# Performance work log

Hardware: AMD Instinct MI355X
Metric: run time of the kernel (lower is better)

## Reference

```python
import jax, jax.numpy as jnp
import numpy as np

B, T, D = 4, 2048, 1024
DK, DV = 1024, 1024
BETA1, BETA2 = 1.0, 1.0
EPS = 1e-12  # torch F.normalize eps


def setup_inputs() -> dict:
    key = jax.random.key(0)
    kx, kq, kk, kv, ko = jax.random.split(key, 5)
    def w(k, shape):
        return jax.random.normal(k, shape, dtype=jnp.float32) * (shape[0] ** -0.5)
    return {
        "x": jax.random.normal(kx, (B, T, D), dtype=jnp.float32),
        # Weights stored [in, out]; torch Linear is x @ W.T with W [out, in] -- equivalent math.
        "Wq": w(kq, (D, DK)),
        "Wk": w(kk, (D, DK)),
        "Wv": w(kv, (D, DV)),
        "Wo": w(ko, (DV, D)),
    }


def reference(x, Wq, Wk, Wv, Wo):
    scale = DK ** -0.5
    q = (x @ Wq) * scale                      # [B,T,DK]
    k = x @ Wk
    k = k / jnp.maximum(jnp.linalg.norm(k, axis=-1, keepdims=True), EPS)
    v = x @ Wv                                # [B,T,DV]
    # time-major for scan
    qT = jnp.swapaxes(q, 0, 1)
    kT = jnp.swapaxes(k, 0, 1)
    vT = jnp.swapaxes(v, 0, 1)
    S0 = jnp.zeros((B, DV, DK), dtype=x.dtype)

    def step(S, qkv_t):
        q_t, k_t, v_t = qkv_t                 # each [B, d]
        # S @ (I - b1 k k^T) = S - b1 (S k) k^T   (same math, rank-1 form)
        Sk = jnp.einsum('bvk,bk->bv', S, k_t)
        S = S - BETA1 * Sk[:, :, None] * k_t[:, None, :] \
              + BETA2 * v_t[:, :, None] * k_t[:, None, :]
        o_t = jnp.einsum('bvk,bk->bv', S, q_t)
        return S, o_t

    _, oT = jax.lax.scan(step, S0, (qT, kT, vT))  # oT: [T,B,DV]
    out = jnp.swapaxes(oT, 0, 1) @ Wo             # [B,T,D]
    return out
```

## Files before the change

kernel.cpp:

```cpp
#include <hip/hip_runtime.h>

typedef unsigned short u16;
typedef __attribute__((ext_vector_type(8))) short short8;
typedef __attribute__((ext_vector_type(4))) float floatx4;

#define B_ 4
#define T_ 2048
#define CH 64

__device__ __forceinline__ u16 f2bf(float f) {
  unsigned int x = __float_as_uint(f);
  return (u16)((x + 0x7FFFu + ((x >> 16) & 1u)) >> 16);
}
__device__ __forceinline__ float bf2f(u16 u) {
  union { unsigned int i; float f; } v; v.i = ((unsigned int)u) << 16; return v.f;
}

__global__ __launch_bounds__(256) void xconv_kernel(const float* __restrict__ x,
                                                    u16* __restrict__ Xbf) {
  size_t idx = ((size_t)blockIdx.x * 256 + threadIdx.x) * 4;
  float4 v = *reinterpret_cast<const float4*>(&x[idx]);
  ushort4 o;
  o.x = f2bf(v.x); o.y = f2bf(v.y); o.z = f2bf(v.z); o.w = f2bf(v.w);
  *reinterpret_cast<ushort4*>(&Xbf[idx]) = o;
}

__global__ __launch_bounds__(256) void wtrans_kernel(
    const float* __restrict__ W0, const float* __restrict__ W1,
    const float* __restrict__ W2, const float* __restrict__ W3,
    u16* __restrict__ T0, u16* __restrict__ T1,
    u16* __restrict__ T2, u16* __restrict__ T3)
{
  const int z = blockIdx.z;
  const float* W = (z == 0) ? W0 : (z == 1) ? W1 : (z == 2) ? W2 : W3;
  u16* T = (z == 0) ? T0 : (z == 1) ? T1 : (z == 2) ? T2 : T3;
  const int k0 = blockIdx.x * 64, n0 = blockIdx.y * 64;
  const int tid = threadIdx.x;
  __shared__ float Tile[64][65];
#pragma unroll
  for (int i = 0; i < 4; ++i) {
    int lin = tid + i * 256;
    int r = lin >> 4, c4 = (lin & 15) * 4;
    *reinterpret_cast<float4*>(&Tile[r][c4]) =
        *reinterpret_cast<const float4*>(&W[(size_t)(k0 + r) * 1024 + n0 + c4]);
  }
  __syncthreads();
#pragma unroll
  for (int i = 0; i < 4; ++i) {
    int lin = tid + i * 256;
    int r = lin >> 4, c4 = (lin & 15) * 4;
    ushort4 o;
    o.x = f2bf(Tile[c4 + 0][r]); o.y = f2bf(Tile[c4 + 1][r]);
    o.z = f2bf(Tile[c4 + 2][r]); o.w = f2bf(Tile[c4 + 3][r]);
    *reinterpret_cast<ushort4*>(&T[(size_t)(n0 + r) * 1024 + k0 + c4]) = o;
  }
}

__global__ __launch_bounds__(256) void mgemm_qkv(
    const u16* __restrict__ Xbf,
    const u16* __restrict__ WqT, const u16* __restrict__ WkT, const u16* __restrict__ WvT,
    u16* __restrict__ Qbf, u16* __restrict__ Kbf, u16* __restrict__ Vbf,
    int tg, int lsh)
{
  const int z = blockIdx.z;
  const u16* BT = (z == 0) ? WqT : ((z == 1) ? WkT : WvT);
  u16* O = (z == 0) ? Qbf : ((z == 1) ? Kbf : Vbf);
  const float scale = (z == 0) ? 0.03125f : 1.0f;
  const int r0 = blockIdx.x * 128, c0 = blockIdx.y * 128;
  const int tid = threadIdx.x;
  const int lane = tid & 63, wave = tid >> 6;
  const int quad = lane >> 4, l16 = lane & 15;
  const int wr = (wave >> 1) * 64, wc = (wave & 1) * 64;

  __shared__ u16 As[128][40];
  __shared__ u16 Bs[128][40];

  const int ar = tid >> 1, ac = (tid & 1) * 16;
  const int lr = r0 + ar;
  const int agrow = ((lr >> lsh) << 11) + tg + (lr & ((1 << lsh) - 1));
  const u16* aptr = &Xbf[(size_t)agrow * 1024 + ac];
  const u16* bptr = &BT[(size_t)(c0 + ar) * 1024 + ac];

  floatx4 acc[4][4] = {};
  for (int k0 = 0; k0 < 1024; k0 += 32) {
    float4 av0 = *reinterpret_cast<const float4*>(aptr + k0);
    float4 av1 = *reinterpret_cast<const float4*>(aptr + k0 + 8);
    float4 bv0 = *reinterpret_cast<const float4*>(bptr + k0);
    float4 bv1 = *reinterpret_cast<const float4*>(bptr + k0 + 8);
    __syncthreads();
    *reinterpret_cast<float4*>(&As[ar][ac]) = av0;
    *reinterpret_cast<float4*>(&As[ar][ac + 8]) = av1;
    *reinterpret_cast<float4*>(&Bs[ar][ac]) = bv0;
    *reinterpret_cast<float4*>(&Bs[ar][ac + 8]) = bv1;
    __syncthreads();
    short8 afr[4], bfr[4];
#pragma unroll
    for (int i = 0; i < 4; ++i) {
      afr[i] = *reinterpret_cast<const short8*>(&As[wr + i * 16 + l16][quad * 8]);
      bfr[i] = *reinterpret_cast<const short8*>(&Bs[wc + i * 16 + l16][quad * 8]);
    }
#pragma unroll
    for (int mi = 0; mi < 4; ++mi)
#pragma unroll
      for (int ni = 0; ni < 4; ++ni)
        acc[mi][ni] = __builtin_amdgcn_mfma_f32_16x16x32_bf16(afr[mi], bfr[ni], acc[mi][ni], 0, 0, 0);
  }
#pragma unroll
  for (int mi = 0; mi < 4; ++mi)
#pragma unroll
    for (int reg = 0; reg < 4; ++reg) {
      int row = r0 + wr + mi * 16 + quad * 4 + reg;
#pragma unroll
      for (int ni = 0; ni < 4; ++ni) {
        int col = c0 + wc + ni * 16 + l16;
        O[(size_t)row * 1024 + col] = f2bf(acc[mi][ni][reg] * scale);
      }
    }
}

__global__ __launch_bounds__(256) void mgemm_out(
    const u16* __restrict__ Obf, const u16* __restrict__ WoT,
    float* __restrict__ out, int tg, int lsh)
{
  const int r0 = blockIdx.x * 128, c0 = blockIdx.y * 128;
  const int tid = threadIdx.x;
  const int lane = tid & 63, wave = tid >> 6;
  const int quad = lane >> 4, l16 = lane & 15;
  const int wr = (wave >> 1) * 64, wc = (wave & 1) * 64;

  __shared__ u16 As[128][40];
  __shared__ u16 Bs[128][40];

  const int ar = tid >> 1, ac = (tid & 1) * 16;
  const u16* aptr = &Obf[(size_t)(r0 + ar) * 1024 + ac];
  const u16* bptr = &WoT[(size_t)(c0 + ar) * 1024 + ac];

  floatx4 acc[4][4] = {};
  for (int k0 = 0; k0 < 1024; k0 += 32) {
    float4 av0 = *reinterpret_cast<const float4*>(aptr + k0);
    float4 av1 = *reinterpret_cast<const float4*>(aptr + k0 + 8);
    float4 bv0 = *reinterpret_cast<const float4*>(bptr + k0);
    float4 bv1 = *reinterpret_cast<const float4*>(bptr + k0 + 8);
    __syncthreads();
    *reinterpret_cast<float4*>(&As[ar][ac]) = av0;
    *reinterpret_cast<float4*>(&As[ar][ac + 8]) = av1;
    *reinterpret_cast<float4*>(&Bs[ar][ac]) = bv0;
    *reinterpret_cast<float4*>(&Bs[ar][ac + 8]) = bv1;
    __syncthreads();
    short8 afr[4], bfr[4];
#pragma unroll
    for (int i = 0; i < 4; ++i) {
      afr[i] = *reinterpret_cast<const short8*>(&As[wr + i * 16 + l16][quad * 8]);
      bfr[i] = *reinterpret_cast<const short8*>(&Bs[wc + i * 16 + l16][quad * 8]);
    }
#pragma unroll
    for (int mi = 0; mi < 4; ++mi)
#pragma unroll
      for (int ni = 0; ni < 4; ++ni)
        acc[mi][ni] = __builtin_amdgcn_mfma_f32_16x16x32_bf16(afr[mi], bfr[ni], acc[mi][ni], 0, 0, 0);
  }
#pragma unroll
  for (int mi = 0; mi < 4; ++mi)
#pragma unroll
    for (int reg = 0; reg < 4; ++reg) {
      int lr = r0 + wr + mi * 16 + quad * 4 + reg;
      int grow = ((lr >> lsh) << 11) + tg + (lr & ((1 << lsh) - 1));
#pragma unroll
      for (int ni = 0; ni < 4; ++ni) {
        int col = c0 + wc + ni * 16 + l16;
        out[(size_t)grow * 1024 + col] = acc[mi][ni][reg];
      }
    }
}

__global__ __launch_bounds__(256) void knorm_kernel(u16* __restrict__ Kbf) {
  const int row = blockIdx.x;
  const int tid = threadIdx.x;
  ushort4 v4 = *reinterpret_cast<const ushort4*>(&Kbf[(size_t)row * 1024 + tid * 4]);
  float a = bf2f(v4.x), b = bf2f(v4.y), c = bf2f(v4.z), d = bf2f(v4.w);
  float ss = a * a + b * b + c * c + d * d;
#pragma unroll
  for (int off = 32; off > 0; off >>= 1) ss += __shfl_down(ss, off);
  __shared__ float wsum[4];
  if ((tid & 63) == 0) wsum[tid >> 6] = ss;
  __syncthreads();
  float tot = wsum[0] + wsum[1] + wsum[2] + wsum[3];
  float inv = 1.0f / fmaxf(sqrtf(tot), 1e-12f);
  ushort4 o;
  o.x = f2bf(a * inv); o.y = f2bf(b * inv); o.z = f2bf(c * inv); o.w = f2bf(d * inv);
  *reinterpret_cast<ushort4*>(&Kbf[(size_t)row * 1024 + tid * 4]) = o;
}

__global__ __launch_bounds__(256) void ktrans_kernel(const u16* __restrict__ Kbf,
                                                     u16* __restrict__ KT,
                                                     int tgs) {
  const int t0 = blockIdx.x * 64;
  const int d0 = blockIdx.y * 64;
  const int b = blockIdx.z;
  const int tid = threadIdx.x;
  __shared__ u16 Tile[64][68];
#pragma unroll
  for (int i = 0; i < 4; ++i) {
    int lin = tid + i * 256;
    int r = lin >> 4, c4 = (lin & 15) * 4;
    *reinterpret_cast<ushort4*>(&Tile[r][c4]) =
        *reinterpret_cast<const ushort4*>(&Kbf[(size_t)(b * tgs + t0 + r) * 1024 + d0 + c4]);
  }
  __syncthreads();
#pragma unroll
  for (int i = 0; i < 4; ++i) {
    int lin = tid + i * 256;
    int r = lin >> 4, c4 = (lin & 15) * 4;
    ushort4 o;
    o.x = Tile[c4 + 0][r]; o.y = Tile[c4 + 1][r];
    o.z = Tile[c4 + 2][r]; o.w = Tile[c4 + 3][r];
    *reinterpret_cast<ushort4*>(&KT[((size_t)b * 1024 + d0 + r) * tgs + t0 + c4]) = o;
  }
}

__global__ __launch_bounds__(256) void attn_winv_kernel(
    const u16* __restrict__ Qbf, const u16* __restrict__ Kbf,
    u16* __restrict__ Pb, u16* __restrict__ Wb, int tgs)
{
  const int cc = blockIdx.x;
  const int b = blockIdx.y;
  const int base = b * tgs + cc * CH;
  const int tid = threadIdx.x;
  const int lane = tid & 63;
  const int wave = tid >> 6;
  const int quad = lane >> 4, l16 = lane & 15;
  const int m0 = wave * 16;

  __shared__ float Asm[64][64];
  __shared__ float Wsm[64][65];

  floatx4 accA[4] = {};
  floatx4 accP[4] = {};
  const u16* arowK = &Kbf[(size_t)(base + m0 + l16) * 1024];
  const u16* arowQ = &Qbf[(size_t)(base + m0 + l16) * 1024];
#pragma unroll 4
  for (int kk = 0; kk < 32; ++kk) {
    short8 aK = *reinterpret_cast<const short8*>(&arowK[kk * 32 + quad * 8]);
    short8 aQ = *reinterpret_cast<const short8*>(&arowQ[kk * 32 + quad * 8]);
#pragma unroll
    for (int nt = 0; nt < 4; ++nt) {
      short8 bK = *reinterpret_cast<const short8*>(
          &Kbf[(size_t)(base + nt * 16 + l16) * 1024 + kk * 32 + quad * 8]);
      accA[nt] = __builtin_amdgcn_mfma_f32_16x16x32_bf16(aK, bK, accA[nt], 0, 0, 0);
      accP[nt] = __builtin_amdgcn_mfma_f32_16x16x32_bf16(aQ, bK, accP[nt], 0, 0, 0);
    }
  }
  const size_t pw0 = ((size_t)(cc * B_ + b) * CH) * 64;
#pragma unroll
  for (int nt = 0; nt < 4; ++nt) {
#pragma unroll
    for (int reg = 0; reg < 4; ++reg) {
      int t = m0 + quad * 4 + reg;
      int i = nt * 16 + l16;
      Asm[t][i] = (i < t) ? accA[nt][reg] : 0.0f;
      Pb[pw0 + (size_t)t * 64 + i] = f2bf((i <= t) ? accP[nt][reg] : 0.0f);
    }
  }
  __syncthreads();

  if (tid < 64) {
    const int j = tid;
    for (int t = 0; t < 64; ++t) {
      float s = (t == j) ? 1.0f : 0.0f;
      for (int i = 0; i < t; ++i) s -= Asm[t][i] * Wsm[i][j];
      Wsm[t][j] = s;
    }
    for (int t = 0; t < 64; ++t)
      Wb[pw0 + (size_t)t * 64 + j] = f2bf(Wsm[t][j]);
  }
}

__global__ __launch_bounds__(512, 2) void chain_kernel(
    const u16* __restrict__ Qbf, const u16* __restrict__ Kbf,
    const u16* __restrict__ KT, const u16* __restrict__ Vbf,
    u16* __restrict__ Obf, const u16* __restrict__ Wb, const u16* __restrict__ Pb,
    float* __restrict__ Sglob, int lsh, int cpg, int g, int ngrp)
{
  const int wg = blockIdx.x;
  const int b = wg >> 6;
  const int sl = wg & 63;
  const int c0 = sl * 16;
  const int tgs = 1 << lsh;
  const int tid = threadIdx.x;
  const int lane = tid & 63;
  const int wave = tid >> 6;
  const int quad = lane >> 4, l16 = lane & 15;
  const int d0w = wave * 128;
  const bool isK = (wave < 4);
  const int m0 = (isK ? wave : (wave - 4)) * 16;

  __shared__ u16 Sb[16][1048];
  __shared__ u16 rhsT[16][88];
  __shared__ u16 uT[16][88];

  floatx4 Sreg[8];
  if (g == 0) {
#pragma unroll
    for (int nt = 0; nt < 8; ++nt) Sreg[nt] = (floatx4){0.f, 0.f, 0.f, 0.f};
    for (int idx = tid; idx < 16 * 256; idx += 512) {
      int r = idx >> 8, d4 = (idx & 255) * 4;
      ushort4 z4 = {0, 0, 0, 0};
      *reinterpret_cast<ushort4*>(&Sb[r][d4]) = z4;
    }
  } else {
#pragma unroll
    for (int nt = 0; nt < 8; ++nt)
#pragma unroll
      for (int reg = 0; reg < 4; ++reg)
        Sreg[nt][reg] = Sglob[((size_t)b * 1024 + c0 + quad * 4 + reg) * 1024 +
                              d0w + nt * 16 + l16];
    for (int idx = tid; idx < 16 * 1024; idx += 512) {
      int r = idx >> 10, d = idx & 1023;
      Sb[r][d] = f2bf(Sglob[((size_t)b * 1024 + c0 + r) * 1024 + d]);
    }
  }
  __syncthreads();

  for (int cc = 0; cc < cpg; ++cc) {
    const int base = b * tgs + cc * CH;
    const size_t pw0 = ((size_t)(cc * B_ + b) * CH) * 64;

    float vv[4];
    if (isK) {
#pragma unroll
      for (int reg = 0; reg < 4; ++reg)
        vv[reg] = bf2f(Vbf[(size_t)(base + m0 + quad * 4 + reg) * 1024 + c0 + l16]);
    }
    short8 wpf0, wpf1;
    {
      const u16* row = (isK ? Wb : Pb) + pw0 + (size_t)(m0 + l16) * 64;
      wpf0 = *reinterpret_cast<const short8*>(row + quad * 8);
      wpf1 = *reinterpret_cast<const short8*>(row + 32 + quad * 8);
    }
    short8 ktf[8][2];
#pragma unroll
    for (int nt = 0; nt < 8; ++nt) {
      const u16* ktrow = &KT[((size_t)b * 1024 + d0w + nt * 16 + l16) * tgs + cc * CH];
      ktf[nt][0] = *reinterpret_cast<const short8*>(ktrow + quad * 8);
      ktf[nt][1] = *reinterpret_cast<const short8*>(ktrow + 32 + quad * 8);
    }

    floatx4 ac0 = {}, ac1 = {}, ac2 = {}, ac3 = {};
    {
      const u16* arow = (isK ? Kbf : Qbf) + (size_t)(base + m0 + l16) * 1024;
#pragma unroll
      for (int kk8 = 0; kk8 < 8; ++kk8) {
        const int kb = kk8 * 4;
        short8 A0 = *reinterpret_cast<const short8*>(&arow[(kb + 0) * 32 + quad * 8]);
        short8 A1 = *reinterpret_cast<const short8*>(&arow[(kb + 1) * 32 + quad * 8]);
        short8 A2 = *reinterpret_cast<const short8*>(&arow[(kb + 2) * 32 + quad * 8]);
        short8 A3 = *reinterpret_cast<const short8*>(&arow[(kb + 3) * 32 + quad * 8]);
        short8 B0 = *reinterpret_cast<const short8*>(&Sb[l16][(kb + 0) * 32 + quad * 8]);
        short8 B1 = *reinterpret_cast<const short8*>(&Sb[l16][(kb + 1) * 32 + quad * 8]);
        short8 B2 = *reinterpret_cast<const short8*>(&Sb[l16][(kb + 2) * 32 + quad * 8]);
        short8 B3 = *reinterpret_cast<const short8*>(&Sb[l16][(kb + 3) * 32 + quad * 8]);
        ac0 = __builtin_amdgcn_mfma_f32_16x16x32_bf16(A0, B0, ac0, 0, 0, 0);
        ac1 = __builtin_amdgcn_mfma_f32_16x16x32_bf16(A1, B1, ac1, 0, 0, 0);
        ac2 = __builtin_amdgcn_mfma_f32_16x16x32_bf16(A2, B2, ac2, 0, 0, 0);
        ac3 = __builtin_amdgcn_mfma_f32_16x16x32_bf16(A3, B3, ac3, 0, 0, 0);
      }
    }
    floatx4 accS = (ac0 + ac1) + (ac2 + ac3);

    if (isK) {
#pragma unroll
      for (int reg = 0; reg < 4; ++reg)
        rhsT[l16][m0 + quad * 4 + reg] = f2bf(vv[reg] - accS[reg]);
    }
    __syncthreads();

    if (isK) {
      floatx4 uacc = {};
      short8 br0 = *reinterpret_cast<const short8*>(&rhsT[l16][quad * 8]);
      short8 br1 = *reinterpret_cast<const short8*>(&rhsT[l16][32 + quad * 8]);
      uacc = __builtin_amdgcn_mfma_f32_16x16x32_bf16(wpf0, br0, uacc, 0, 0, 0);
      uacc = __builtin_amdgcn_mfma_f32_16x16x32_bf16(wpf1, br1, uacc, 0, 0, 0);
#pragma unroll
      for (int reg = 0; reg < 4; ++reg)
        uT[l16][m0 + quad * 4 + reg] = f2bf(uacc[reg]);
    }
    __syncthreads();

    if (!isK) {
      floatx4 oacc = accS;
      short8 bu0 = *reinterpret_cast<const short8*>(&uT[l16][quad * 8]);
      short8 bu1 = *reinterpret_cast<const short8*>(&uT[l16][32 + quad * 8]);
      oacc = __builtin_amdgcn_mfma_f32_16x16x32_bf16(wpf0, bu0, oacc, 0, 0, 0);
      oacc = __builtin_amdgcn_mfma_f32_16x16x32_bf16(wpf1, bu1, oacc, 0, 0, 0);
#pragma unroll
      for (int reg = 0; reg < 4; ++reg) {
        int t = m0 + quad * 4 + reg;
        Obf[(size_t)(base + t) * 1024 + c0 + l16] = f2bf(oacc[reg]);
      }
    }

    {
      short8 ua0 = *reinterpret_cast<const short8*>(&uT[l16][quad * 8]);
      short8 ua1 = *reinterpret_cast<const short8*>(&uT[l16][32 + quad * 8]);
#pragma unroll
      for (int nt = 0; nt < 8; ++nt) {
        floatx4 cf = Sreg[nt];
        cf = __builtin_amdgcn_mfma_f32_16x16x32_bf16(ua0, ktf[nt][0], cf, 0, 0, 0);
        cf = __builtin_amdgcn_mfma_f32_16x16x32_bf16(ua1, ktf[nt][1], cf, 0, 0, 0);
        Sreg[nt] = cf;
        const int dn = d0w + nt * 16;
#pragma unroll
        for (int reg = 0; reg < 4; ++reg)
          Sb[quad * 4 + reg][dn + l16] = f2bf(cf[reg]);
      }
    }
    __syncthreads();
  }

  if (g < ngrp - 1) {
#pragma unroll
    for (int nt = 0; nt < 8; ++nt)
#pragma unroll
      for (int reg = 0; reg < 4; ++reg)
        Sglob[((size_t)b * 1024 + c0 + quad * 4 + reg) * 1024 + d0w + nt * 16 + l16] =
            Sreg[nt][reg];
  }
}

extern "C" void kernel_launch(void* const* d_in, const int* in_sizes, int n_in,
                              void* d_out, int out_size, void* d_ws, size_t ws_size,
                              hipStream_t stream) {
  const float* x  = (const float*)d_in[0];
  const float* Wq = (const float*)d_in[1];
  const float* Wk = (const float*)d_in[2];
  const float* Wv = (const float*)d_in[3];
  const float* Wo = (const float*)d_in[4];
  float* out = (float*)d_out;

  int lsh = 8;
  {
    const int cand[4] = {11, 10, 9, 8};
    for (int i = 0; i < 4; ++i) {
      size_t tgs = (size_t)1 << cand[i];
      size_t C = (size_t)B_ * tgs * 1024;
      size_t cpg = tgs / CH;
      size_t need = (size_t)B_ * T_ * 1024 * 2
                  + 4 * ((size_t)1024 * 1024 * 2)
                  + 5 * (C * 2)
                  + 2 * (cpg * B_ * CH * 64 * 2)
                  + (size_t)B_ * 1024 * 1024 * 4
                  + 32768;
      if (need <= ws_size) { lsh = cand[i]; break; }
    }
  }
  const int tgs = 1 << lsh;
  const int cpg = tgs / CH;
  const int ngrp = T_ / tgs;
  const int rows = B_ * tgs;

  char* ws = (char*)d_ws;
  size_t off = 0;
  auto alloc = [&](size_t bytes) -> void* {
    void* p = ws + off;
    off += (bytes + 255) & ~(size_t)255;
    return p;
  };
  u16* Xbf = (u16*)alloc((size_t)B_ * T_ * 1024 * 2);
  u16* WqT = (u16*)alloc((size_t)1024 * 1024 * 2);
  u16* WkT = (u16*)alloc((size_t)1024 * 1024 * 2);
  u16* WvT = (u16*)alloc((size_t)1024 * 1024 * 2);
  u16* WoT = (u16*)alloc((size_t)1024 * 1024 * 2);
  u16* Qbf = (u16*)alloc((size_t)rows * 1024 * 2);
  u16* Kbf = (u16*)alloc((size_t)rows * 1024 * 2);
  u16* Vbf = (u16*)alloc((size_t)rows * 1024 * 2);
  u16* KT  = (u16*)alloc((size_t)rows * 1024 * 2);
  u16* Obf = (u16*)alloc((size_t)rows * 1024 * 2);
  u16* Pb  = (u16*)alloc((size_t)cpg * B_ * CH * 64 * 2);
  u16* Wb  = (u16*)alloc((size_t)cpg * B_ * CH * 64 * 2);
  float* Sglob = (float*)alloc((size_t)B_ * 1024 * 1024 * 4);

  xconv_kernel<<<B_ * T_, 256, 0, stream>>>(x, Xbf);
  wtrans_kernel<<<dim3(16, 16, 4), 256, 0, stream>>>(Wq, Wk, Wv, Wo, WqT, WkT, WvT, WoT);

  for (int g = 0; g < ngrp; ++g) {
    int tg = g * tgs;
    mgemm_qkv<<<dim3(rows / 128, 8, 3), 256, 0, stream>>>(Xbf, WqT, WkT, WvT,
                                                          Qbf, Kbf, Vbf, tg, lsh);
    knorm_kernel<<<rows, 256, 0, stream>>>(Kbf);
    ktrans_kernel<<<dim3(tgs / 64, 16, B_), 256, 0, stream>>>(Kbf, KT, tgs);
    attn_winv_kernel<<<dim3(cpg, B_), 256, 0, stream>>>(Qbf, Kbf, Pb, Wb, tgs);
    chain_kernel<<<256, 512, 0, stream>>>(Qbf, Kbf, KT, Vbf, Obf, Wb, Pb, Sglob,
                                          lsh, cpg, g, ngrp);
    mgemm_out<<<dim3(rows / 128, 8), 256, 0, stream>>>(Obf, WoT, out, tg, lsh);
  }
}
```

Measured before the change: 638.1 us.

## Software-pipeline A-row loads and interleave KT loads in chain kernel

The chain kernel now prefetches the next group of Q/K A-fragments one iteration ahead, carrying them across chunk boundaries, and spreads the KT fragment loads through the MFMA loop. This hides global-load latency behind the matrix ops. The __syncthreads calls become raw s_waitcnt lgkmcnt(0) + s_barrier, so barriers no longer wait on outstanding vector-memory loads. Workgroup-to-(batch, slice) mapping is also changed to interleave batches across consecutive block IDs. The cost is higher register pressure from the prefetch buffers, and the barriers now depend on the hand-written inline asm being correct.

Result: no change. 642.6 us (+0.7%).

```diff
diff --git a/kernel.cpp b/kernel.cpp
--- a/kernel.cpp
+++ b/kernel.cpp
@@ -14,6 +14,10 @@
 }
 __device__ __forceinline__ float bf2f(u16 u) {
   union { unsigned int i; float f; } v; v.i = ((unsigned int)u) << 16; return v.f;
+}
+
+__device__ __forceinline__ void barrier_lgkm() {
+  asm volatile("s_waitcnt lgkmcnt(0)\n\ts_barrier" ::: "memory");
 }
 
 __global__ __launch_bounds__(256) void xconv_kernel(const float* __restrict__ x,
@@ -282,8 +286,9 @@
     float* __restrict__ Sglob, int lsh, int cpg, int g, int ngrp)
 {
   const int wg = blockIdx.x;
-  const int b = wg >> 6;
-  const int sl = wg & 63;
+  const int t8 = wg & 7;
+  const int b = t8 >> 1;
+  const int sl = ((wg >> 3) << 1) | (t8 & 1);
   const int c0 = sl * 16;
   const int tgs = 1 << lsh;
   const int tid = threadIdx.x;
@@ -321,6 +326,13 @@
   }
   __syncthreads();
 
+  const u16* const Abase = isK ? Kbf : Qbf;
+  const u16* arow = Abase + (size_t)(b * tgs + m0 + l16) * 1024;
+  short8 pa0 = *reinterpret_cast<const short8*>(arow + 0 * 32 + quad * 8);
+  short8 pa1 = *reinterpret_cast<const short8*>(arow + 1 * 32 + quad * 8);
+  short8 pa2 = *reinterpret_cast<const short8*>(arow + 2 * 32 + quad * 8);
+  short8 pa3 = *reinterpret_cast<const short8*>(arow + 3 * 32 + quad * 8);
+
   for (int cc = 0; cc < cpg; ++cc) {
     const int base = b * tgs + cc * CH;
     const size_t pw0 = ((size_t)(cc * B_ + b) * CH) * 64;
@@ -337,42 +349,47 @@
       wpf0 = *reinterpret_cast<const short8*>(row + quad * 8);
       wpf1 = *reinterpret_cast<const short8*>(row + 32 + quad * 8);
     }
+
     short8 ktf[8][2];
-#pragma unroll
-    for (int nt = 0; nt < 8; ++nt) {
-      const u16* ktrow = &KT[((size_t)b * 1024 + d0w + nt * 16 + l16) * tgs + cc * CH];
-      ktf[nt][0] = *reinterpret_cast<const short8*>(ktrow + quad * 8);
-      ktf[nt][1] = *reinterpret_cast<const short8*>(ktrow + 32 + quad * 8);
-    }
-
     floatx4 ac0 = {}, ac1 = {}, ac2 = {}, ac3 = {};
-    {
-      const u16* arow = (isK ? Kbf : Qbf) + (size_t)(base + m0 + l16) * 1024;
-#pragma unroll
-      for (int kk8 = 0; kk8 < 8; ++kk8) {
-        const int kb = kk8 * 4;
-        short8 A0 = *reinterpret_cast<const short8*>(&arow[(kb + 0) * 32 + quad * 8]);
-        short8 A1 = *reinterpret_cast<const short8*>(&arow[(kb + 1) * 32 + quad * 8]);
-        short8 A2 = *reinterpret_cast<const short8*>(&arow[(kb + 2) * 32 + quad * 8]);
-        short8 A3 = *reinterpret_cast<const short8*>(&arow[(kb + 3) * 32 + quad * 8]);
-        short8 B0 = *reinterpret_cast<const short8*>(&Sb[l16][(kb + 0) * 32 + quad * 8]);
-        short8 B1 = *reinterpret_cast<const short8*>(&Sb[l16][(kb + 1) * 32 + quad * 8]);
-        short8 B2 = *reinterpret_cast<const short8*>(&Sb[l16][(kb + 2) * 32 + quad * 8]);
-        short8 B3 = *reinterpret_cast<const short8*>(&Sb[l16][(kb + 3) * 32 + quad * 8]);
-        ac0 = __builtin_amdgcn_mfma_f32_16x16x32_bf16(A0, B0, ac0, 0, 0, 0);
-        ac1 = __builtin_amdgcn_mfma_f32_16x16x32_bf16(A1, B1, ac1, 0, 0, 0);
-        ac2 = __builtin_amdgcn_mfma_f32_16x16x32_bf16(A2, B2, ac2, 0, 0, 0);
-        ac3 = __builtin_amdgcn_mfma_f32_16x16x32_bf16(A3, B3, ac3, 0, 0, 0);
+#pragma unroll
+    for (int kk8 = 0; kk8 < 8; ++kk8) {
+      const int kb = kk8 * 4;
+      {
+        const u16* ktrow = &KT[((size_t)b * 1024 + d0w + kk8 * 16 + l16) * tgs + cc * CH];
+        ktf[kk8][0] = *reinterpret_cast<const short8*>(ktrow + quad * 8);
+        ktf[kk8][1] = *reinterpret_cast<const short8*>(ktrow + 32 + quad * 8);
       }
+      const u16* nap = (kk8 < 7) ? (arow + (kb + 4) * 32)
+                                 : (arow + (cc + 1 < cpg ? CH * 1024 : 0));
+      short8 na0 = *reinterpret_cast<const short8*>(nap + 0 * 32 + quad * 8);
+      short8 na1 = *reinterpret_cast<const short8*>(nap + 1 * 32 + quad * 8);
+      short8 na2 = *reinterpret_cast<const short8*>(nap + 2 * 32 + quad * 8);
+      short8 na3 = *reinterpret_cast<const short8*>(nap + 3 * 32 + quad * 8);
+      short8 b0 = *reinterpret_cast<const short8*>(&Sb[l16][(kb + 0) * 32 + quad * 8]);
+      short8 b1 = *reinterpret_cast<const short8*>(&Sb[l16][(kb + 1) * 32 + quad * 8]);
+      short8 b2 = *reinterpret_cast<const short8*>(&Sb[l16][(kb + 2) * 32 + quad * 8]);
+      short8 b3 = *reinterpret_cast<const short8*>(&Sb[l16][(kb + 3) * 32 + quad * 8]);
+      ac0 = __builtin_amdgcn_mfma_f32_16x16x32_bf16(pa0, b0, ac0, 0, 0, 0);
+      ac1 = __builtin_amdgcn_mfma_f32_16x16x32_bf16(pa1, b1, ac1, 0, 0, 0);
+      ac2 = __builtin_amdgcn_mfma_f32_16x16x32_bf16(pa2, b2, ac2, 0, 0, 0);
+      ac3 = __builtin_amdgcn_mfma_f32_16x16x32_bf16(pa3, b3, ac3, 0, 0, 0);
+      pa0 = na0; pa1 = na1; pa2 = na2; pa3 = na3;
     }
     floatx4 accS = (ac0 + ac1) + (ac2 + ac3);
+
+    asm volatile("" ::
+      "v"(ktf[0][0]), "v"(ktf[0][1]), "v"(ktf[1][0]), "v"(ktf[1][1]),
+      "v"(ktf[2][0]), "v"(ktf[2][1]), "v"(ktf[3][0]), "v"(ktf[3][1]),
+      "v"(ktf[4][0]), "v"(ktf[4][1]), "v"(ktf[5][0]), "v"(ktf[5][1]),
+      "v"(ktf[6][0]), "v"(ktf[6][1]), "v"(ktf[7][0]), "v"(ktf[7][1]));
 
     if (isK) {
 #pragma unroll
       for (int reg = 0; reg < 4; ++reg)
         rhsT[l16][m0 + quad * 4 + reg] = f2bf(vv[reg] - accS[reg]);
     }
-    __syncthreads();
+    barrier_lgkm();
 
     if (isK) {
       floatx4 uacc = {};
@@ -384,7 +401,7 @@
       for (int reg = 0; reg < 4; ++reg)
         uT[l16][m0 + quad * 4 + reg] = f2bf(uacc[reg]);
     }
-    __syncthreads();
+    barrier_lgkm();
 
     if (!isK) {
       floatx4 oacc = accS;
@@ -414,7 +431,8 @@
           Sb[quad * 4 + reg][dn + l16] = f2bf(cf[reg]);
       }
     }
-    __syncthreads();
+    barrier_lgkm();
+    arow += CH * 1024;
   }
 
   if (g < ngrp - 1) {
```

## Double chunk size in sequential chain by composing two 64-step inverses into 128

Applied to the files above, without the earlier changes.

The precompute stage now also forms cross-chunk K·K^T and Q·K^T blocks for adjacent 64-step chunks. A new kernel composes them into 128x128 block-triangular inverse (W128) and attention (P128) matrices. The chain kernel then advances the recurrent state 128 steps per iteration instead of 64, which halves the number of serial state updates and barriers. Other changes swap __syncthreads for a raw lgkmcnt barrier, remap workgroups to interleave batches, and skip the Sglob buffer when only one group is used. The cost is an extra kernel launch, more intermediate buffers, and bf16 rounding of the composed inverse.

Measured after the change: 702.0 us. 10.0% more time.

```diff
diff --git a/kernel.cpp b/kernel.cpp
--- a/kernel.cpp
+++ b/kernel.cpp
@@ -6,7 +6,6 @@
 
 #define B_ 4
 #define T_ 2048
-#define CH 64
 
 __device__ __forceinline__ u16 f2bf(float f) {
   unsigned int x = __float_as_uint(f);
@@ -14,6 +13,10 @@
 }
 __device__ __forceinline__ float bf2f(u16 u) {
   union { unsigned int i; float f; } v; v.i = ((unsigned int)u) << 16; return v.f;
+}
+
+__device__ __forceinline__ void barrier_lgkm() {
+  asm volatile("s_waitcnt lgkmcnt(0)\n\ts_barrier" ::: "memory");
 }
 
 __global__ __launch_bounds__(256) void xconv_kernel(const float* __restrict__ x,
@@ -220,11 +223,13 @@
 
 __global__ __launch_bounds__(256) void attn_winv_kernel(
     const u16* __restrict__ Qbf, const u16* __restrict__ Kbf,
-    u16* __restrict__ Pb, u16* __restrict__ Wb, int tgs)
+    u16* __restrict__ Pb, u16* __restrict__ Wb, u16* __restrict__ WbT,
+    u16* __restrict__ Mb, u16* __restrict__ Nb, int tgs)
 {
   const int cc = blockIdx.x;
   const int b = blockIdx.y;
-  const int base = b * tgs + cc * CH;
+  const int base = b * tgs + cc * 64;
+  const int basep = base - (cc > 0 ? 64 : 0);
   const int tid = threadIdx.x;
   const int lane = tid & 63;
   const int wave = tid >> 6;
@@ -236,9 +241,11 @@
 
   floatx4 accA[4] = {};
   floatx4 accP[4] = {};
+  floatx4 accM[4] = {};
+  floatx4 accN[4] = {};
   const u16* arowK = &Kbf[(size_t)(base + m0 + l16) * 1024];
   const u16* arowQ = &Qbf[(size_t)(base + m0 + l16) * 1024];
-#pragma unroll 4
+#pragma unroll 2
   for (int kk = 0; kk < 32; ++kk) {
     short8 aK = *reinterpret_cast<const short8*>(&arowK[kk * 32 + quad * 8]);
     short8 aQ = *reinterpret_cast<const short8*>(&arowQ[kk * 32 + quad * 8]);
@@ -249,8 +256,17 @@
       accA[nt] = __builtin_amdgcn_mfma_f32_16x16x32_bf16(aK, bK, accA[nt], 0, 0, 0);
       accP[nt] = __builtin_amdgcn_mfma_f32_16x16x32_bf16(aQ, bK, accP[nt], 0, 0, 0);
     }
-  }
-  const size_t pw0 = ((size_t)(cc * B_ + b) * CH) * 64;
+    if (cc > 0) {
+#pragma unroll
+      for (int nt = 0; nt < 4; ++nt) {
+        short8 bKp = *reinterpret_cast<const short8*>(
+            &Kbf[(size_t)(basep + nt * 16 + l16) * 1024 + kk * 32 + quad * 8]);
+        accM[nt] = __builtin_amdgcn_mfma_f32_16x16x32_bf16(aK, bKp, accM[nt], 0, 0, 0);
+        accN[nt] = __builtin_amdgcn_mfma_f32_16x16x32_bf16(aQ, bKp, accN[nt], 0, 0, 0);
+      }
+    }
+  }
+  const size_t pw0 = ((size_t)(cc * B_ + b) * 64) * 64;
 #pragma unroll
   for (int nt = 0; nt < 4; ++nt) {
 #pragma unroll
@@ -259,6 +275,8 @@
       int i = nt * 16 + l16;
       Asm[t][i] = (i < t) ? accA[nt][reg] : 0.0f;
       Pb[pw0 + (size_t)t * 64 + i] = f2bf((i <= t) ? accP[nt][reg] : 0.0f);
+      Mb[pw0 + (size_t)t * 64 + i] = f2bf(accM[nt][reg]);
+      Nb[pw0 + (size_t)t * 64 + i] = f2bf(accN[nt][reg]);
     }
   }
   __syncthreads();
@@ -270,20 +288,92 @@
       for (int i = 0; i < t; ++i) s -= Asm[t][i] * Wsm[i][j];
       Wsm[t][j] = s;
     }
-    for (int t = 0; t < 64; ++t)
-      Wb[pw0 + (size_t)t * 64 + j] = f2bf(Wsm[t][j]);
-  }
+    for (int t = 0; t < 64; ++t) {
+      u16 w = f2bf(Wsm[t][j]);
+      Wb[pw0 + (size_t)t * 64 + j] = w;
+      WbT[pw0 + (size_t)j * 64 + t] = w;
+    }
+  }
+}
+
+__global__ __launch_bounds__(256) void wcomp_kernel(
+    const u16* __restrict__ Pb, const u16* __restrict__ Wb,
+    const u16* __restrict__ WbT, const u16* __restrict__ Mb,
+    const u16* __restrict__ Nb,
+    u16* __restrict__ W128, u16* __restrict__ P128)
+{
+  const int c1 = blockIdx.x;
+  const int b = blockIdx.y;
+  const int cc1 = 2 * c1, cc2 = 2 * c1 + 1;
+  const size_t pw1 = ((size_t)(cc1 * B_ + b)) * 4096;
+  const size_t pw2 = ((size_t)(cc2 * B_ + b)) * 4096;
+  const size_t pwX = ((size_t)(c1 * B_ + b)) * 16384;
+  const int tid = threadIdx.x;
+  const int lane = tid & 63, wave = tid >> 6;
+  const int quad = lane >> 4, l16 = lane & 15;
+  const int m0 = wave * 16;
+
+  __shared__ u16 XT[64][72];
+
+  floatx4 xacc[4] = {};
+#pragma unroll
+  for (int kk = 0; kk < 2; ++kk) {
+    short8 mf = *reinterpret_cast<const short8*>(
+        &Mb[pw2 + (size_t)(m0 + l16) * 64 + kk * 32 + quad * 8]);
+#pragma unroll
+    for (int nt = 0; nt < 4; ++nt) {
+      short8 w1tf = *reinterpret_cast<const short8*>(
+          &WbT[pw1 + (size_t)(nt * 16 + l16) * 64 + kk * 32 + quad * 8]);
+      xacc[nt] = __builtin_amdgcn_mfma_f32_16x16x32_bf16(mf, w1tf, xacc[nt], 0, 0, 0);
+    }
+  }
+#pragma unroll
+  for (int nt = 0; nt < 4; ++nt)
+#pragma unroll
+    for (int reg = 0; reg < 4; ++reg)
+      XT[nt * 16 + l16][m0 + quad * 4 + reg] = f2bf(xacc[nt][reg]);
+
+  for (int idx = tid; idx < 4096; idx += 256) {
+    int t = idx >> 6, j = idx & 63;
+    W128[pwX + (size_t)t * 128 + j]            = Wb[pw1 + (size_t)t * 64 + j];
+    W128[pwX + (size_t)t * 128 + 64 + j]       = 0;
+    W128[pwX + (size_t)(64 + t) * 128 + 64 + j] = Wb[pw2 + (size_t)t * 64 + j];
+    P128[pwX + (size_t)t * 128 + j]            = Pb[pw1 + (size_t)t * 64 + j];
+    P128[pwX + (size_t)t * 128 + 64 + j]       = 0;
+    P128[pwX + (size_t)(64 + t) * 128 + j]     = Nb[pw2 + (size_t)t * 64 + j];
+    P128[pwX + (size_t)(64 + t) * 128 + 64 + j] = Pb[pw2 + (size_t)t * 64 + j];
+  }
+  __syncthreads();
+
+  floatx4 facc[4] = {};
+#pragma unroll
+  for (int kk = 0; kk < 2; ++kk) {
+    short8 w2f = *reinterpret_cast<const short8*>(
+        &Wb[pw2 + (size_t)(m0 + l16) * 64 + kk * 32 + quad * 8]);
+#pragma unroll
+    for (int nt = 0; nt < 4; ++nt) {
+      short8 xtf = *reinterpret_cast<const short8*>(&XT[nt * 16 + l16][kk * 32 + quad * 8]);
+      facc[nt] = __builtin_amdgcn_mfma_f32_16x16x32_bf16(w2f, xtf, facc[nt], 0, 0, 0);
+    }
+  }
+#pragma unroll
+  for (int nt = 0; nt < 4; ++nt)
+#pragma unroll
+    for (int reg = 0; reg < 4; ++reg)
+      W128[pwX + (size_t)(64 + m0 + quad * 4 + reg) * 128 + nt * 16 + l16] =
+          f2bf(-facc[nt][reg]);
 }
 
 __global__ __launch_bounds__(512, 2) void chain_kernel(
     const u16* __restrict__ Qbf, const u16* __restrict__ Kbf,
     const u16* __restrict__ KT, const u16* __restrict__ Vbf,
-    u16* __restrict__ Obf, const u16* __restrict__ Wb, const u16* __restrict__ Pb,
+    u16* __restrict__ Obf, const u16* __restrict__ W128, const u16* __restrict__ P128,
     float* __restrict__ Sglob, int lsh, int cpg, int g, int ngrp)
 {
   const int wg = blockIdx.x;
-  const int b = wg >> 6;
-  const int sl = wg & 63;
+  const int t8 = wg & 7;
+  const int b = t8 >> 1;
+  const int sl = ((wg >> 3) << 1) | (t8 & 1);
   const int c0 = sl * 16;
   const int tgs = 1 << lsh;
   const int tid = threadIdx.x;
@@ -295,8 +385,8 @@
   const int m0 = (isK ? wave : (wave - 4)) * 16;
 
   __shared__ u16 Sb[16][1048];
-  __shared__ u16 rhsT[16][88];
-  __shared__ u16 uT[16][88];
+  __shared__ u16 rhsT[16][136];
+  __shared__ u16 uT[16][136];
 
   floatx4 Sreg[8];
   if (g == 0) {
@@ -321,92 +411,110 @@
   }
   __syncthreads();
 
+  const u16* const Abase = isK ? Kbf : Qbf;
+  const u16* const WPb   = isK ? W128 : P128;
+
   for (int cc = 0; cc < cpg; ++cc) {
-    const int base = b * tgs + cc * CH;
-    const size_t pw0 = ((size_t)(cc * B_ + b) * CH) * 64;
-
-    float vv[4];
+    const int base = b * tgs + cc * 128;
+    const size_t pw = ((size_t)(cc * B_ + b)) * 16384;
+    const u16* arowa = Abase + (size_t)(base + m0 + l16) * 1024 + quad * 8;
+    const u16* arowb = arowa + (size_t)64 * 1024;
+
+    floatx4 aa0 = {}, aa1 = {}, aa2 = {}, aa3 = {};
+    floatx4 ab0 = {}, ab1 = {}, ab2 = {}, ab3 = {};
+#pragma unroll
+    for (int kk8 = 0; kk8 < 8; ++kk8) {
+      const int kb = kk8 * 4;
+      short8 fa0 = *reinterpret_cast<const short8*>(arowa + (kb + 0) * 32);
+      short8 fa1 = *reinterpret_cast<const short8*>(arowa + (kb + 1) * 32);
+      short8 fa2 = *reinterpret_cast<const short8*>(arowa + (kb + 2) * 32);
+      short8 fa3 = *reinterpret_cast<const short8*>(arowa + (kb + 3) * 32);
+      short8 fb0 = *reinterpret_cast<const short8*>(arowb + (kb + 0) * 32);
+      short8 fb1 = *reinterpret_cast<const short8*>(arowb + (kb + 1) * 32);
+      short8 fb2 = *reinterpret_cast<const short8*>(arowb + (kb + 2) * 32);
+      short8 fb3 = *reinterpret_cast<const short8*>(arowb + (kb + 3) * 32);
+      short8 s0 = *reinterpret_cast<const short8*>(&Sb[l16][(kb + 0) * 32 + quad * 8]);
+      short8 s1 = *reinterpret_cast<const short8*>(&Sb[l16][(kb + 1) * 32 + quad * 8]);
+      short8 s2 = *reinterpret_cast<const short8*>(&Sb[l16][(kb + 2) * 32 + quad * 8]);
+      short8 s3 = *reinterpret_cast<const short8*>(&Sb[l16][(kb + 3) * 32 + quad * 8]);
+      aa0 = __builtin_amdgcn_mfma_f32_16x16x32_bf16(fa0, s0, aa0, 0, 0, 0);
+      ab0 = __builtin_amdgcn_mfma_f32_16x16x32_bf16(fb0, s0, ab0, 0, 0, 0);
+      aa1 = __builtin_amdgcn_mfma_f32_16x16x32_bf16(fa1, s1, aa1, 0, 0, 0);
+      ab1 = __builtin_amdgcn_mfma_f32_16x16x32_bf16(fb1, s1, ab1, 0, 0, 0);
+      aa2 = __builtin_amdgcn_mfma_f32_16x16x32_bf16(fa2, s2, aa2, 0, 0, 0);
+      ab2 = __builtin_amdgcn_mfma_f32_16x16x32_bf16(fb2, s2, ab2, 0, 0, 0);
+      aa3 = __builtin_amdgcn_mfma_f32_16x16x32_bf16(fa3, s3, aa3, 0, 0, 0);
+      ab3 = __builtin_amdgcn_mfma_f32_16x16x32_bf16(fb3, s3, ab3, 0, 0, 0);
+    }
+    floatx4 accSa = (aa0 + aa1) + (aa2 + aa3);
+    floatx4 accSb = (ab0 + ab1) + (ab2 + ab3);
+
     if (isK) {
 #pragma unroll
-      for (int reg = 0; reg < 4; ++reg)
-        vv[reg] = bf2f(Vbf[(size_t)(base + m0 + quad * 4 + reg) * 1024 + c0 + l16]);
-    }
-    short8 wpf0, wpf1;
+      for (int reg = 0; reg < 4; ++reg) {
+        int ra = base + m0 + quad * 4 + reg;
+        rhsT[l16][m0 + quad * 4 + reg] =
+            f2bf(bf2f(Vbf[(size_t)ra * 1024 + c0 + l16]) - accSa[reg]);
+        rhsT[l16][64 + m0 + quad * 4 + reg] =
+            f2bf(bf2f(Vbf[(size_t)(ra + 64) * 1024 + c0 + l16]) - accSb[reg]);
+      }
+    }
+    barrier_lgkm();
+
+    if (isK) {
+      const u16* wra = WPb + pw + (size_t)(m0 + l16) * 128 + quad * 8;
+      const u16* wrb = wra + (size_t)64 * 128;
+      floatx4 ua = {}, ub = {};
+#pragma unroll
+      for (int f = 0; f < 4; ++f) {
+        short8 br = *reinterpret_cast<const short8*>(&rhsT[l16][f * 32 + quad * 8]);
+        short8 wa = *reinterpret_cast<const short8*>(wra + f * 32);
+        short8 wb = *reinterpret_cast<const short8*>(wrb + f * 32);
+        ua = __builtin_amdgcn_mfma_f32_16x16x32_bf16(wa, br, ua, 0, 0, 0);
+        ub = __builtin_amdgcn_mfma_f32_16x16x32_bf16(wb, br, ub, 0, 0, 0);
+      }
+#pragma unroll
+      for (int reg = 0; reg < 4; ++reg) {
+        uT[l16][m0 + quad * 4 + reg] = f2bf(ua[reg]);
+        uT[l16][64 + m0 + quad * 4 + reg] = f2bf(ub[reg]);
+      }
+    }
+    barrier_lgkm();
+
+    if (!isK) {
+      const u16* pra = WPb + pw + (size_t)(m0 + l16) * 128 + quad * 8;
+      const u16* prb = pra + (size_t)64 * 128;
+      floatx4 oa = accSa, ob = accSb;
+#pragma unroll
+      for (int f = 0; f < 4; ++f) {
+        short8 bu = *reinterpret_cast<const short8*>(&uT[l16][f * 32 + quad * 8]);
+        short8 pa = *reinterpret_cast<const short8*>(pra + f * 32);
+        short8 pb = *reinterpret_cast<const short8*>(prb + f * 32);
+        oa = __builtin_amdgcn_mfma_f32_16x16x32_bf16(pa, bu, oa, 0, 0, 0);
+        ob = __builtin_amdgcn_mfma_f32_16x16x32_bf16(pb, bu, ob, 0, 0, 0);
+      }
+#pragma unroll
+      for (int reg = 0; reg < 4; ++reg) {
+        int ra = base + m0 + quad * 4 + reg;
+        Obf[(size_t)ra * 1024 + c0 + l16] = f2bf(oa[reg]);
+        Obf[(size_t)(ra + 64) * 1024 + c0 + l16] = f2bf(ob[reg]);
+      }
+    }
+
     {
-      const u16* row = (isK ? Wb : Pb) + pw0 + (size_t)(m0 + l16) * 64;
-      wpf0 = *reinterpret_cast<const short8*>(row + quad * 8);
-      wpf1 = *reinterpret_cast<const short8*>(row + 32 + quad * 8);
-    }
-    short8 ktf[8][2];
-#pragma unroll
-    for (int nt = 0; nt < 8; ++nt) {
-      const u16* ktrow = &KT[((size_t)b * 1024 + d0w + nt * 16 + l16) * tgs + cc * CH];
-      ktf[nt][0] = *reinterpret_cast<const short8*>(ktrow + quad * 8);
-      ktf[nt][1] = *reinterpret_cast<const short8*>(ktrow + 32 + quad * 8);
-    }
-
-    floatx4 ac0 = {}, ac1 = {}, ac2 = {}, ac3 = {};
-    {
-      const u16* arow = (isK ? Kbf : Qbf) + (size_t)(base + m0 + l16) * 1024;
-#pragma unroll
-      for (int kk8 = 0; kk8 < 8; ++kk8) {
-        const int kb = kk8 * 4;
-        short8 A0 = *reinterpret_cast<const short8*>(&arow[(kb + 0) * 32 + quad * 8]);
-        short8 A1 = *reinterpret_cast<const short8*>(&arow[(kb + 1) * 32 + quad * 8]);
-        short8 A2 = *reinterpret_cast<const short8*>(&arow[(kb + 2) * 32 + quad * 8]);
-        short8 A3 = *reinterpret_cast<const short8*>(&arow[(kb + 3) * 32 + quad * 8]);
-        short8 B0 = *reinterpret_cast<const short8*>(&Sb[l16][(kb + 0) * 32 + quad * 8]);
-        short8 B1 = *reinterpret_cast<const short8*>(&Sb[l16][(kb + 1) * 32 + quad * 8]);
-        short8 B2 = *reinterpret_cast<const short8*>(&Sb[l16][(kb + 2) * 32 + quad * 8]);
-        short8 B3 = *reinterpret_cast<const short8*>(&Sb[l16][(kb + 3) * 32 + quad * 8]);
-        ac0 = __builtin_amdgcn_mfma_f32_16x16x32_bf16(A0, B0, ac0, 0, 0, 0);
-        ac1 = __builtin_amdgcn_mfma_f32_16x16x32_bf16(A1, B1, ac1, 0, 0, 0);
-        ac2 = __builtin_amdgcn_mfma_f32_16x16x32_bf16(A2, B2, ac2, 0, 0, 0);
-        ac3 = __builtin_amdgcn_mfma_f32_16x16x32_bf16(A3, B3, ac3, 0, 0, 0);
-      }
-    }
-    floatx4 accS = (ac0 + ac1) + (ac2 + ac3);
-
-    if (isK) {
-#pragma unroll
-      for (int reg = 0; reg < 4; ++reg)
-        rhsT[l16][m0 + quad * 4 + reg] = f2bf(vv[reg] - accS[reg]);
-    }
-    __syncthreads();
-
-    if (isK) {
-      floatx4 uacc = {};
-      short8 br0 = *reinterpret_cast<const short8*>(&rhsT[l16][quad * 8]);
-      short8 br1 = *reinterpret_cast<const short8*>(&rhsT[l16][32 + quad * 8]);
-      uacc = __builtin_amdgcn_mfma_f32_16x16x32_bf16(wpf0, br0, uacc, 0, 0, 0);
-      uacc = __builtin_amdgcn_mfma_f32_16x16x32_bf16(wpf1, br1, uacc, 0, 0, 0);
-#pragma unroll
-      for (int reg = 0; reg < 4; ++reg)
-        uT[l16][m0 + quad * 4 + reg] = f2bf(uacc[reg]);
-    }
-    __syncthreads();
-
-    if (!isK) {
-      floatx4 oacc = accS;
-      short8 bu0 = *reinterpret_cast<const short8*>(&uT[l16][quad * 8]);
-      short8 bu1 = *reinterpret_cast<const short8*>(&uT[l16][32 + quad * 8]);
-      oacc = __builtin_amdgcn_mfma_f32_16x16x32_bf16(wpf0, bu0, oacc, 0, 0, 0);
-      oacc = __builtin_amdgcn_mfma_f32_16x16x32_bf16(wpf1, bu1, oacc, 0, 0, 0);
-#pragma unroll
-      for (int reg = 0; reg < 4; ++reg) {
-        int t = m0 + quad * 4 + reg;
-        Obf[(size_t)(base + t) * 1024 + c0 + l16] = f2bf(oacc[reg]);
-      }
-    }
-
-    {
-      short8 ua0 = *reinterpret_cast<const short8*>(&uT[l16][quad * 8]);
-      short8 ua1 = *reinterpret_cast<const short8*>(&uT[l16][32 + quad * 8]);
+      short8 uf0 = *reinterpret_cast<const short8*>(&uT[l16][0 * 32 + quad * 8]);
+      short8 uf1 = *reinterpret_cast<const short8*>(&uT[l16][1 * 32 + quad * 8]);
+      short8 uf2 = *reinterpret_cast<const short8*>(&uT[l16][2 * 32 + quad * 8]);
+      short8 uf3 = *reinterpret_cast<const short8*>(&uT[l16][3 * 32 + quad * 8]);
+      const u16* ktb = KT + ((size_t)b * 1024 + d0w + l16) * tgs + (size_t)cc * 128 + quad * 8;
 #pragma unroll
       for (int nt = 0; nt < 8; ++nt) {
+        const u16* kr = ktb + (size_t)(nt * 16) * tgs;
         floatx4 cf = Sreg[nt];
-        cf = __builtin_amdgcn_mfma_f32_16x16x32_bf16(ua0, ktf[nt][0], cf, 0, 0, 0);
-        cf = __builtin_amdgcn_mfma_f32_16x16x32_bf16(ua1, ktf[nt][1], cf, 0, 0, 0);
+        cf = __builtin_amdgcn_mfma_f32_16x16x32_bf16(uf0, *reinterpret_cast<const short8*>(kr + 0),  cf, 0, 0, 0);
+        cf = __builtin_amdgcn_mfma_f32_16x16x32_bf16(uf1, *reinterpret_cast<const short8*>(kr + 32), cf, 0, 0, 0);
+        cf = __builtin_amdgcn_mfma_f32_16x16x32_bf16(uf2, *reinterpret_cast<const short8*>(kr + 64), cf, 0, 0, 0);
+        cf = __builtin_amdgcn_mfma_f32_16x16x32_bf16(uf3, *reinterpret_cast<const short8*>(kr + 96), cf, 0, 0, 0);
         Sreg[nt] = cf;
         const int dn = d0w + nt * 16;
 #pragma unroll
@@ -414,7 +522,7 @@
           Sb[quad * 4 + reg][dn + l16] = f2bf(cf[reg]);
       }
     }
-    __syncthreads();
+    barrier_lgkm();
   }
 
   if (g < ngrp - 1) {
@@ -443,18 +551,21 @@
     for (int i = 0; i < 4; ++i) {
       size_t tgs = (size_t)1 << cand[i];
       size_t C = (size_t)B_ * tgs * 1024;
-      size_t cpg = tgs / CH;
+      size_t c64 = tgs / 64, c128 = tgs / 128;
+      int ng = T_ / (int)tgs;
       size_t need = (size_t)B_ * T_ * 1024 * 2
                   + 4 * ((size_t)1024 * 1024 * 2)
                   + 5 * (C * 2)
-                  + 2 * (cpg * B_ * CH * 64 * 2)
-                  + (size_t)B_ * 1024 * 1024 * 4
+                  + 5 * (c64 * B_ * 4096 * 2)
+                  + 2 * (c128 * B_ * 16384 * 2)
+                  + (ng > 1 ? (size_t)B_ * 1024 * 1024 * 4 : 0)
                   + 32768;
       if (need <= ws_size) { lsh = cand[i]; break; }
     }
   }
   const int tgs = 1 << lsh;
-  const int cpg = tgs / CH;
+  const int cpg64 = tgs / 64;
+  const int cpg128 = tgs / 128;
   const int ngrp = T_ / tgs;
   const int rows = B_ * tgs;
 
@@ -475,9 +586,15 @@
   u16* Vbf = (u16*)alloc((size_t)rows * 1024 * 2);
   u16* KT  = (u16*)alloc((size_t)rows * 1024 * 2);
   u16* Obf = (u16*)alloc((size_t)rows * 1024 * 2);
-  u16* Pb  = (u16*)alloc((size_t)cpg * B_ * CH * 64 * 2);
-  u16* Wb  = (u16*)alloc((size_t)cpg * B_ * CH * 64 * 2);
-  float* Sglob = (float*)alloc((size_t)B_ * 1024 * 1024 * 4);
+  u16* Pb  = (u16*)alloc((size_t)cpg64 * B_ * 4096 * 2);
+  u16* Wb  = (u16*)alloc((size_t)cpg64 * B_ * 4096 * 2);
+  u16* WbT = (u16*)alloc((size_t)cpg64 * B_ * 4096 * 2);
+  u16* Mb  = (u16*)alloc((size_t)cpg64 * B_ * 4096 * 2);
+  u16* Nb  = (u16*)alloc((size_t)cpg64 * B_ * 4096 * 2);
+  u16* W128 = (u16*)alloc((size_t)cpg128 * B_ * 16384 * 2);
+  u16* P128 = (u16*)alloc((size_t)cpg128 * B_ * 16384 * 2);
+  float* Sglob = (ngrp > 1) ? (float*)alloc((size_t)B_ * 1024 * 1024 * 4)
+                            : (float*)ws;
 
   xconv_kernel<<<B_ * T_, 256, 0, stream>>>(x, Xbf);
   wtrans_kernel<<<dim3(16, 16, 4), 256, 0, stream>>>(Wq, Wk, Wv, Wo, WqT, WkT, WvT, WoT);
@@ -488,9 +605,12 @@
                                                           Qbf, Kbf, Vbf, tg, lsh);
     knorm_kernel<<<rows, 256, 0, stream>>>(Kbf);
     ktrans_kernel<<<dim3(tgs / 64, 16, B_), 256, 0, stream>>>(Kbf, KT, tgs);
-    attn_winv_kernel<<<dim3(cpg, B_), 256, 0, stream>>>(Qbf, Kbf, Pb, Wb, tgs);
-    chain_kernel<<<256, 512, 0, stream>>>(Qbf, Kbf, KT, Vbf, Obf, Wb, Pb, Sglob,
-                                          lsh, cpg, g, ngrp);
+    attn_winv_kernel<<<dim3(cpg64, B_), 256, 0, stream>>>(Qbf, Kbf, Pb, Wb, WbT,
+                                                          Mb, Nb, tgs);
+    wcomp_kernel<<<dim3(cpg128, B_), 256, 0, stream>>>(Pb, Wb, WbT, Mb, Nb,
+                                                       W128, P128);
+    chain_kernel<<<256, 512, 0, stream>>>(Qbf, Kbf, KT, Vbf, Obf, W128, P128,
+                                          Sglob, lsh, cpg128, g, ngrp);
     mgemm_out<<<dim3(rows / 128, 8), 256, 0, stream>>>(Obf, WoT, out, tg, lsh);
   }
 }
```
